# Kernel optimization log

Measured on AMD Instinct MI355X. Metric: run time of the kernel, lower is better.

Reference implementation:

```python
import jax, jax.numpy as jnp
import numpy as np

B, T = 64, 64
HUMAN, IN = 64, 8
HS, ES, K = 1024, 1024, 7
PSI_H, PSI_LR = 1024, 30

_PAR_SHAPES = [(HS, HS), (HS,), (IN, HS), (HS, HUMAN), (IN, HUMAN - IN)]
_PAR_SIZES = [int(np.prod(s)) for s in _PAR_SHAPES]
N_PSI = int(sum(_PAR_SIZES))
_OFFS = np.cumsum([0] + _PAR_SIZES)


def setup_inputs() -> dict:
    key = jax.random.key(0)
    ks = jax.random.split(key, 16)
    def xav(k, shape):
        lim = float(np.sqrt(6.0 / (shape[0] + shape[1])))
        return jax.random.uniform(k, shape, minval=-lim, maxval=lim, dtype=jnp.float32)
    def uni(k, shape, s):
        return jax.random.uniform(k, shape, minval=-s, maxval=s, dtype=jnp.float32)
    se = float(1.0 / np.sqrt(ES))
    return {
        "inputs": jax.random.normal(ks[0], (B, T, IN), jnp.float32),
        "outputs": jax.random.normal(ks[1], (B, T, HUMAN), jnp.float32),
        "eps": jax.random.normal(ks[2], (B, K), jnp.float32),
        "enc_Wih": uni(ks[3], (3 * ES, HUMAN), se),
        "enc_Whh": uni(ks[4], (3 * ES, ES), se),
        "enc_bih": uni(ks[5], (3 * ES,), se),
        "enc_bhh": uni(ks[6], (3 * ES,), se),
        "to_mu": xav(ks[7], (ES, K)),
        "to_lsigma": xav(ks[8], (ES, K)),
        "to_lsigma_bias": -0.5 * jnp.ones((K,), jnp.float32),
        "W1": xav(ks[9], (K, PSI_H)),
        "b1": jnp.zeros((PSI_H,), jnp.float32),
        "W2": xav(ks[10], (PSI_H, PSI_LR)),
        "b2": jnp.zeros((PSI_LR,), jnp.float32),
        "W3": xav(ks[11], (PSI_LR, N_PSI)),
        "b3": jnp.zeros((N_PSI,), jnp.float32),
        "gru_Wih": xav(ks[12], (IN, 2 * HS)),
        "gru_Whh": xav(ks[13], (HS, 2 * HS)),
        "gru_bias": jnp.concatenate([jnp.zeros((HS,)), jnp.ones((HS,))]).astype(jnp.float32),
    }


def _gru_cell(h, x, Wih, Whh, bih, bhh):
    # torch.nn.GRUCell math, gate order (r, z, n)
    gx = x @ Wih.T + bih
    gh = h @ Whh.T + bhh
    xr, xz, xn = jnp.split(gx, 3, axis=-1)
    hr, hz, hn = jnp.split(gh, 3, axis=-1)
    r = jax.nn.sigmoid(xr + hr)
    z = jax.nn.sigmoid(xz + hz)
    n = jnp.tanh(xn + r * hn)
    return (1.0 - z) * n + z * h


def _split_psi(psi):
    # psi: [B, N_PSI] -> per-sample (Whh, bh, Wih, C, D)
    return [psi[:, _OFFS[i]:_OFFS[i + 1]].reshape((-1,) + _PAR_SHAPES[i]) for i in range(5)]


def reference(inputs, outputs, eps, enc_Wih, enc_Whh, enc_bih, enc_bhh,
              to_mu, to_lsigma, to_lsigma_bias, W1, b1, W2, b2, W3, b3,
              gru_Wih, gru_Whh, gru_bias):
    bsz = inputs.shape[0]
    # ---- encoder: GRUCell over time-major outputs ----
    out_tm = jnp.swapaxes(outputs, 0, 1)  # [T, B, HUMAN]
    h0 = jnp.zeros((bsz, ES), inputs.dtype)
    h_enc = _gru_cell(h0, out_tm[0], enc_Wih, enc_Whh, enc_bih, enc_bhh)
    def enc_step(h, x):
        h = _gru_cell(h, x, enc_Wih, enc_Whh, enc_bih, enc_bhh)
        return h, None
    h_enc, _ = jax.lax.scan(enc_step, h_enc, out_tm[1:])
    mu = h_enc @ to_mu                       # [B, K]
    logstd = h_enc @ to_lsigma + to_lsigma_bias
    z = mu + eps * jnp.exp(logstd)
    # ---- hypernetwork psi decoder ----
    psi = (jnp.tanh(z @ W1 + b1) @ W2 + b2) @ W3 + b3   # [B, N_PSI]
    Whh_b, bh_b, Wih_b, C_b, D_b = _split_psi(psi)
    # ---- per-sample GRU decoder, vectorized over batch, scan over time ----
    gx_all = jnp.einsum('bti,ij->tbj', inputs, gru_Wih)  # [T, B, 2*HS]
    xW_all = jnp.einsum('bti,bih->tbh', inputs, Wih_b)   # [T, B, HS]

    def dec_step(h, xs):
        gx_t, xW_t = xs
        pre = gx_t + h @ gru_Whh + gru_bias   # [B, 2*HS]
        z_t = jax.nn.sigmoid(pre[:, :HS])
        r_t = jax.nn.sigmoid(pre[:, HS:])
        hWhh = jnp.einsum('bh,bhk->bk', h, Whh_b) + bh_b
        eta = jnp.tanh(xW_t + r_t * jnp.tanh(hWhh))
        h_new = z_t * h + (1.0 - z_t) * eta
        return h_new, h_new

    state0 = jnp.zeros((bsz, HS), inputs.dtype)
    h_last, dec_seq = jax.lax.scan(dec_step, state0, (gx_all, xW_all))
    dec_seq = jnp.swapaxes(dec_seq, 0, 1)    # [B, T, HS]
    # ---- readout ----
    yhats = jnp.einsum('bth,bhm->btm', dec_seq, C_b)
    xD = jnp.einsum('bti,bim->btm', inputs, D_b)  # [B, T, HUMAN-IN]
    yhats = yhats + jnp.concatenate([jnp.zeros_like(inputs), xD], axis=-1)
    # residual output
    yhats = yhats + jnp.concatenate(
        [inputs, jnp.zeros((bsz, inputs.shape[1], HUMAN - IN), inputs.dtype)], axis=-1)
    states = jax.lax.stop_gradient(h_last)
    return yhats, mu, logstd, states
```

## Files before the change

### kernel.cpp

```cpp
#include <hip/hip_runtime.h>

namespace {
constexpr int nT = 64;
constexpr int nK = 7;
constexpr long N_PSI = 1123776;
constexpr long SZ_WHH = 1048576;
constexpr long REST_SZ = 75200;
constexpr long R_BH = 0;
constexpr long R_WIH = 1024;
constexpr long R_C = 9216;
constexpr long R_D = 74752;
constexpr int NCH = 16;
constexpr int CHR = 64;
constexpr long PHALF = (long)NCH * 64 * 1024;
}

typedef __attribute__((ext_vector_type(4))) unsigned short us4;
typedef __attribute__((ext_vector_type(2))) unsigned short us2;

__device__ __forceinline__ float b2f(unsigned short u) {
  return __uint_as_float(((unsigned int)u) << 16);
}
__device__ __forceinline__ unsigned short f2b(float f) {
  unsigned int u = __float_as_uint(f);
  return (unsigned short)((u + 0x7fffu + ((u >> 16) & 1u)) >> 16);
}
__device__ __forceinline__ float sigm(float x) { return 1.f / (1.f + __expf(-x)); }

__global__ void transpose_bf16_k(const float* __restrict__ in, unsigned short* __restrict__ out,
                                 int rows, int cols) {
  __shared__ float tile[32][33];
  int x = blockIdx.x * 32 + threadIdx.x;
  int y = blockIdx.y * 32 + threadIdx.y;
  #pragma unroll
  for (int i = 0; i < 32; i += 8)
    if ((y + i) < rows && x < cols) tile[threadIdx.y + i][threadIdx.x] = in[(long)(y + i) * cols + x];
  __syncthreads();
  x = blockIdx.y * 32 + threadIdx.x;
  y = blockIdx.x * 32 + threadIdx.y;
  #pragma unroll
  for (int i = 0; i < 32; i += 8)
    if ((y + i) < cols && x < rows) out[(long)(y + i) * rows + x] = f2b(tile[threadIdx.x][threadIdx.y + i]);
}

__global__ void cvt_bf16_k(const float* __restrict__ in, unsigned short* __restrict__ out, long n) {
  long i = (long)blockIdx.x * 256 + threadIdx.x;
  if (i < n) out[i] = f2b(in[i]);
}

__global__ __launch_bounds__(256) void enc_gx_k(const float* __restrict__ outputs,
                                                const unsigned short* __restrict__ WtWihB,
                                                const float* __restrict__ bih,
                                                unsigned short* __restrict__ gxE) {
  int g0 = blockIdx.x * 256;
  int btg = blockIdx.y;
  __shared__ unsigned short ws[64 * 256];
  __shared__ float xs[64][64];
  for (int i = threadIdx.x; i < 64 * 256; i += 256)
    ws[i] = WtWihB[(long)(i >> 8) * 3072 + g0 + (i & 255)];
  for (int i = threadIdx.x; i < 64 * 64; i += 256) {
    int idx = btg * 64 + (i >> 6);
    int t = idx >> 6, b = idx & 63;
    xs[i >> 6][i & 63] = outputs[((long)b * nT + t) * 64 + (i & 63)];
  }
  __syncthreads();
  float bihv = bih[g0 + threadIdx.x];
  for (int j = 0; j < 64; ++j) {
    int idx = btg * 64 + j;
    float acc = bihv;
    #pragma unroll 8
    for (int i = 0; i < 64; ++i) acc += xs[j][i] * b2f(ws[i * 256 + threadIdx.x]);
    gxE[(long)idx * 3072 + g0 + threadIdx.x] = f2b(acc);
  }
}

__global__ __launch_bounds__(256) void dec_gx_k(const float* __restrict__ inputs,
                                                const float* __restrict__ gWih,
                                                const float* __restrict__ gbias,
                                                unsigned short* __restrict__ gxD) {
  int g0 = blockIdx.x * 256;
  int btg = blockIdx.y;
  __shared__ float ws[8][256];
  __shared__ float xs[64][8];
  for (int i = threadIdx.x; i < 8 * 256; i += 256)
    ws[i >> 8][i & 255] = gWih[(long)(i >> 8) * 2048 + g0 + (i & 255)];
  for (int i = threadIdx.x; i < 64 * 8; i += 256) {
    int idx = btg * 64 + (i >> 3);
    int t = idx >> 6, b = idx & 63;
    xs[i >> 3][i & 7] = inputs[((long)b * nT + t) * 8 + (i & 7)];
  }
  __syncthreads();
  float bv = gbias[g0 + threadIdx.x];
  for (int j = 0; j < 64; ++j) {
    int idx = btg * 64 + j;
    float acc = bv;
    #pragma unroll
    for (int i = 0; i < 8; ++i) acc += xs[j][i] * ws[i][threadIdx.x];
    gxD[(long)idx * 2048 + g0 + threadIdx.x] = f2b(acc);
  }
}

__global__ __launch_bounds__(256) void xW_k(const float* __restrict__ inputs,
                                            const float* __restrict__ Rest,
                                            unsigned short* __restrict__ xWb) {
  int k0 = blockIdx.x * 256;
  int b = blockIdx.y;
  __shared__ float ws[8][256];
  __shared__ float xs[64][8];
  const float* RB = Rest + (long)b * REST_SZ + R_WIH;
  for (int i = threadIdx.x; i < 8 * 256; i += 256)
    ws[i >> 8][i & 255] = RB[(long)(i >> 8) * 1024 + k0 + (i & 255)];
  for (int i = threadIdx.x; i < 64 * 8; i += 256)
    xs[i >> 3][i & 7] = inputs[((long)b * nT + (i >> 3)) * 8 + (i & 7)];
  __syncthreads();
  for (int t = 0; t < 64; ++t) {
    float acc = 0.f;
    #pragma unroll
    for (int i = 0; i < 8; ++i) acc += xs[t][i] * ws[i][threadIdx.x];
    xWb[((long)t * 64 + b) * 1024 + k0 + threadIdx.x] = f2b(acc);
  }
}

__global__ __launch_bounds__(256) void enc_step_k(
    const unsigned short* __restrict__ W,
    const unsigned short* __restrict__ gxE,
    const float* __restrict__ bhh,
    float* __restrict__ hEnc,
    const float* __restrict__ pRr, const float* __restrict__ pZr, const float* __restrict__ pNr,
    float* __restrict__ pRw, float* __restrict__ pZw, float* __restrict__ pNw,
    int t) {
  int c = blockIdx.x & (NCH - 1);
  int sp = blockIdx.x >> 4;
  int b0 = sp * 2, b1 = b0 + 1;
  __shared__ float h0s[CHR], h1s[CHR];

  int v = threadIdx.x;
  if (v < 2 * CHR) {
    int hi = v >> 6;
    int bb = hi ? b1 : b0;
    int e = c * CHR + (v & 63);
    float sr = 0.f, sz = 0.f, sn = 0.f;
    if (t > 0) {
      #pragma unroll
      for (int cc = 0; cc < NCH; ++cc) {
        long base = ((long)cc * 64 + bb) * 1024 + e;
        sr += pRr[base]; sz += pZr[base]; sn += pNr[base];
      }
    }
    long gb = ((long)t * 64 + bb) * 3072;
    float xr = b2f(gxE[gb + e]), xz = b2f(gxE[gb + 1024 + e]), xn = b2f(gxE[gb + 2048 + e]);
    float hr = sr + bhh[e], hz = sz + bhh[1024 + e], hn = sn + bhh[2048 + e];
    float r = sigm(xr + hr);
    float z = sigm(xz + hz);
    float n = tanhf(xn + r * hn);
    float hold = (t > 0) ? hEnc[(long)bb * 1024 + e] : 0.f;
    float hnew = (1.f - z) * n + z * hold;
    hEnc[(long)bb * 1024 + e] = hnew;
    if (hi) h1s[v & 63] = hnew; else h0s[v & 63] = hnew;
  }
  __syncthreads();

  if (t < nT - 1) {
    int e0 = threadIdx.x * 4;
    float ar0[4] = {}, az0[4] = {}, an0[4] = {}, ar1[4] = {}, az1[4] = {}, an1[4] = {};
    const unsigned short* Wb = W + (long)(c * CHR) * 3072 + e0;
    #pragma unroll 4
    for (int j = 0; j < CHR; ++j) {
      us4 wr = *(const us4*)(Wb + (long)j * 3072);
      us4 wz = *(const us4*)(Wb + (long)j * 3072 + 1024);
      us4 wn = *(const us4*)(Wb + (long)j * 3072 + 2048);
      float hv0 = h0s[j], hv1 = h1s[j];
      #pragma unroll
      for (int q = 0; q < 4; ++q) {
        float fr = b2f(wr[q]), fz = b2f(wz[q]), fn = b2f(wn[q]);
        ar0[q] += hv0 * fr; az0[q] += hv0 * fz; an0[q] += hv0 * fn;
        ar1[q] += hv1 * fr; az1[q] += hv1 * fz; an1[q] += hv1 * fn;
      }
    }
    long i0 = ((long)c * 64 + b0) * 1024 + e0;
    long i1 = i0 + 1024;
    *(float4*)(pRw + i0) = make_float4(ar0[0], ar0[1], ar0[2], ar0[3]);
    *(float4*)(pZw + i0) = make_float4(az0[0], az0[1], az0[2], az0[3]);
    *(float4*)(pNw + i0) = make_float4(an0[0], an0[1], an0[2], an0[3]);
    *(float4*)(pRw + i1) = make_float4(ar1[0], ar1[1], ar1[2], ar1[3]);
    *(float4*)(pZw + i1) = make_float4(az1[0], az1[1], az1[2], az1[3]);
    *(float4*)(pNw + i1) = make_float4(an1[0], an1[1], an1[2], an1[3]);
  }
}

__global__ __launch_bounds__(256) void latent_hyper_k(
    const float* __restrict__ h_enc,
    const float* __restrict__ to_mu, const float* __restrict__ to_lsig,
    const float* __restrict__ lsig_bias, const float* __restrict__ eps,
    const float* __restrict__ W1, const float* __restrict__ b1,
    const float* __restrict__ W2, const float* __restrict__ b2,
    float* __restrict__ out_mu, float* __restrict__ out_lsig,
    float* __restrict__ a2out) {
  int b = blockIdx.x;
  __shared__ float hs[1024];
  __shared__ float zv[8];
  __shared__ float a1[1024];
  for (int i = threadIdx.x; i < 1024; i += 256) hs[i] = h_enc[b * 1024 + i];
  __syncthreads();
  int g = threadIdx.x >> 5, s = threadIdx.x & 31;
  if (g < nK) {
    float am = 0.f, as_ = 0.f;
    for (int h = s; h < 1024; h += 32) {
      float hv = hs[h];
      am += hv * to_mu[h * nK + g];
      as_ += hv * to_lsig[h * nK + g];
    }
    #pragma unroll
    for (int m = 16; m >= 1; m >>= 1) { am += __shfl_xor(am, m); as_ += __shfl_xor(as_, m); }
    if (s == 0) {
      float ls = as_ + lsig_bias[g];
      out_mu[b * nK + g] = am;
      out_lsig[b * nK + g] = ls;
      zv[g] = am + eps[b * nK + g] * __expf(ls);
    }
  }
  __syncthreads();
  for (int j = threadIdx.x; j < 1024; j += 256) {
    float acc = b1[j];
    #pragma unroll
    for (int i = 0; i < nK; ++i) acc += zv[i] * W1[i * 1024 + j];
    a1[j] = tanhf(acc);
  }
  __syncthreads();
  int l = threadIdx.x >> 3, s8 = threadIdx.x & 7;
  if (l < 30) {
    float acc = 0.f;
    for (int j = s8; j < 1024; j += 8) acc += a1[j] * W2[j * 30 + l];
    acc += __shfl_xor(acc, 4);
    acc += __shfl_xor(acc, 2);
    acc += __shfl_xor(acc, 1);
    if (s8 == 0) a2out[b * 30 + l] = acc + b2[l];
  }
}

__global__ __launch_bounds__(256) void psi_k(const float* __restrict__ a2,
                                             const float* __restrict__ W3, const float* __restrict__ b3,
                                             unsigned short* __restrict__ WhhB, float* __restrict__ Rest) {
  __shared__ float sa[64 * 30];
  for (int i = threadIdx.x; i < 64 * 30; i += 256) sa[i] = a2[i];
  long n0 = ((long)blockIdx.x * 256 + threadIdx.x) * 2;
  __syncthreads();
  if (n0 >= N_PSI) return;
  float2 w[30];
  #pragma unroll
  for (int l = 0; l < 30; ++l) w[l] = *(const float2*)(W3 + (long)l * N_PSI + n0);
  float2 bb = *(const float2*)(b3 + n0);
  bool isWhh = (n0 < SZ_WHH);
  for (int b = 0; b < 64; ++b) {
    float a0 = bb.x, a1v = bb.y;
    const float* ab = &sa[b * 30];
    #pragma unroll
    for (int l = 0; l < 30; ++l) { float av = ab[l]; a0 += av * w[l].x; a1v += av * w[l].y; }
    if (isWhh) {
      us2 o; o[0] = f2b(a0); o[1] = f2b(a1v);
      *(us2*)(WhhB + (long)b * SZ_WHH + n0) = o;
    } else {
      *(float2*)(Rest + (long)b * REST_SZ + (n0 - SZ_WHH)) = make_float2(a0, a1v);
    }
  }
}

__global__ __launch_bounds__(256) void wmax_k(const unsigned short* __restrict__ WhhB,
                                              float* __restrict__ pmax) {
  int b = blockIdx.x >> 2, rq = blockIdx.x & 3;
  int k0 = threadIdx.x * 4;
  float m0 = 0.f, m1 = 0.f, m2 = 0.f, m3 = 0.f;
  const unsigned short* W = WhhB + (long)b * SZ_WHH + (long)rq * 256 * 1024 + k0;
  #pragma unroll 4
  for (int j = 0; j < 256; ++j) {
    us4 w = *(const us4*)(W + (long)j * 1024);
    m0 = fmaxf(m0, fabsf(b2f(w[0])));
    m1 = fmaxf(m1, fabsf(b2f(w[1])));
    m2 = fmaxf(m2, fabsf(b2f(w[2])));
    m3 = fmaxf(m3, fabsf(b2f(w[3])));
  }
  *(float4*)(pmax + ((long)b * 4 + rq) * 1024 + k0) = make_float4(m0, m1, m2, m3);
}

__global__ __launch_bounds__(256) void wscale_k(const float* __restrict__ pmax,
                                                float* __restrict__ wsc) {
  int b = blockIdx.x;
  int k0 = threadIdx.x * 4;
  float4 a = *(const float4*)(pmax + ((long)b * 4 + 0) * 1024 + k0);
  float4 c = *(const float4*)(pmax + ((long)b * 4 + 1) * 1024 + k0);
  float4 d = *(const float4*)(pmax + ((long)b * 4 + 2) * 1024 + k0);
  float4 e = *(const float4*)(pmax + ((long)b * 4 + 3) * 1024 + k0);
  float m0 = fmaxf(fmaxf(a.x, c.x), fmaxf(d.x, e.x));
  float m1 = fmaxf(fmaxf(a.y, c.y), fmaxf(d.y, e.y));
  float m2 = fmaxf(fmaxf(a.z, c.z), fmaxf(d.z, e.z));
  float m3 = fmaxf(fmaxf(a.w, c.w), fmaxf(d.w, e.w));
  float s0 = (m0 > 0.f) ? m0 / 127.f : 1.f;
  float s1 = (m1 > 0.f) ? m1 / 127.f : 1.f;
  float s2 = (m2 > 0.f) ? m2 / 127.f : 1.f;
  float s3 = (m3 > 0.f) ? m3 / 127.f : 1.f;
  *(float4*)(wsc + (long)b * 1024 + k0) = make_float4(s0, s1, s2, s3);
}

__global__ __launch_bounds__(256) void wquant_k(const unsigned short* __restrict__ WhhB,
                                                const float* __restrict__ wsc,
                                                char* __restrict__ Q8) {
  int b = blockIdx.x >> 2, rq = blockIdx.x & 3;
  int k0 = threadIdx.x * 4;
  float4 s = *(const float4*)(wsc + (long)b * 1024 + k0);
  float i0 = 1.f / s.x, i1 = 1.f / s.y, i2 = 1.f / s.z, i3 = 1.f / s.w;
  const unsigned short* W = WhhB + (long)b * SZ_WHH + (long)rq * 256 * 1024 + k0;
  char* Q = Q8 + (long)b * SZ_WHH + (long)rq * 256 * 1024 + k0;
  #pragma unroll 4
  for (int j = 0; j < 256; ++j) {
    us4 w = *(const us4*)(W + (long)j * 1024);
    int q0 = __float2int_rn(b2f(w[0]) * i0);
    int q1 = __float2int_rn(b2f(w[1]) * i1);
    int q2 = __float2int_rn(b2f(w[2]) * i2);
    int q3 = __float2int_rn(b2f(w[3]) * i3);
    q0 = min(127, max(-127, q0)); q1 = min(127, max(-127, q1));
    q2 = min(127, max(-127, q2)); q3 = min(127, max(-127, q3));
    *(char4*)(Q + (long)j * 1024) = make_char4((char)q0, (char)q1, (char)q2, (char)q3);
  }
}

__global__ __launch_bounds__(256) void dec_step_q8_k(
    const char* __restrict__ Q8,
    const float* __restrict__ Wsc,
    const unsigned short* __restrict__ gWhhB,
    const unsigned short* __restrict__ gxD,
    const unsigned short* __restrict__ xWb,
    const float* __restrict__ Rest,
    float* __restrict__ decS,
    const float* __restrict__ pZr, const float* __restrict__ pRr, const float* __restrict__ pWr,
    float* __restrict__ pZw, float* __restrict__ pRw, float* __restrict__ pWw,
    int t) {
  int c = blockIdx.x & (NCH - 1);
  int sp = blockIdx.x >> 4;
  int b0 = sp * 2, b1 = b0 + 1;
  __shared__ float h0s[CHR], h1s[CHR];

  int v = threadIdx.x;
  if (v < 2 * CHR) {
    int hi = v >> 6;
    int bb = hi ? b1 : b0;
    int k = c * CHR + (v & 63);
    float sz = 0.f, sr = 0.f, sw = 0.f;
    float hold = 0.f;
    if (t > 0) {
      #pragma unroll
      for (int cc = 0; cc < NCH; ++cc) {
        long base = ((long)cc * 64 + bb) * 1024 + k;
        sz += pZr[base]; sr += pRr[base]; sw += pWr[base];
      }
      hold = decS[((long)bb * nT + (t - 1)) * 1024 + k];
    }
    long gb = ((long)t * 64 + bb) * 2048;
    float gz = b2f(gxD[gb + k]), gr = b2f(gxD[gb + 1024 + k]);
    float z = sigm(gz + sz);
    float r = sigm(gr + sr);
    float hW = sw + Rest[(long)bb * REST_SZ + R_BH + k];
    float xw = b2f(xWb[((long)t * 64 + bb) * 1024 + k]);
    float eta = tanhf(xw + r * tanhf(hW));
    float hnew = z * hold + (1.f - z) * eta;
    decS[((long)bb * nT + t) * 1024 + k] = hnew;
    if (hi) h1s[v & 63] = hnew; else h0s[v & 63] = hnew;
  }
  __syncthreads();

  if (t < nT - 1) {
    int k0 = threadIdx.x * 4;
    float az0[4] = {}, ar0[4] = {}, aw0[4] = {}, az1[4] = {}, ar1[4] = {}, aw1[4] = {};
    const unsigned short* G = gWhhB + (long)(c * CHR) * 2048 + k0;
    const char* Q0 = Q8 + (long)b0 * SZ_WHH + (long)(c * CHR) * 1024 + k0;
    const char* Q1 = Q8 + (long)b1 * SZ_WHH + (long)(c * CHR) * 1024 + k0;
    #pragma unroll 4
    for (int j = 0; j < CHR; ++j) {
      us4 wz = *(const us4*)(G + (long)j * 2048);
      us4 wr = *(const us4*)(G + (long)j * 2048 + 1024);
      char4 q0 = *(const char4*)(Q0 + (long)j * 1024);
      char4 q1 = *(const char4*)(Q1 + (long)j * 1024);
      float hv0 = h0s[j], hv1 = h1s[j];
      float f00 = (float)q0.x, f01 = (float)q0.y, f02 = (float)q0.z, f03 = (float)q0.w;
      float f10 = (float)q1.x, f11 = (float)q1.y, f12 = (float)q1.z, f13 = (float)q1.w;
      #pragma unroll
      for (int q = 0; q < 4; ++q) {
        float fz = b2f(wz[q]), fr = b2f(wr[q]);
        az0[q] += hv0 * fz; ar0[q] += hv0 * fr;
        az1[q] += hv1 * fz; ar1[q] += hv1 * fr;
      }
      aw0[0] += hv0 * f00; aw0[1] += hv0 * f01; aw0[2] += hv0 * f02; aw0[3] += hv0 * f03;
      aw1[0] += hv1 * f10; aw1[1] += hv1 * f11; aw1[2] += hv1 * f12; aw1[3] += hv1 * f13;
    }
    float4 s0v = *(const float4*)(Wsc + (long)b0 * 1024 + k0);
    float4 s1v = *(const float4*)(Wsc + (long)b1 * 1024 + k0);
    aw0[0] *= s0v.x; aw0[1] *= s0v.y; aw0[2] *= s0v.z; aw0[3] *= s0v.w;
    aw1[0] *= s1v.x; aw1[1] *= s1v.y; aw1[2] *= s1v.z; aw1[3] *= s1v.w;
    long i0 = ((long)c * 64 + b0) * 1024 + k0;
    long i1 = i0 + 1024;
    *(float4*)(pZw + i0) = make_float4(az0[0], az0[1], az0[2], az0[3]);
    *(float4*)(pRw + i0) = make_float4(ar0[0], ar0[1], ar0[2], ar0[3]);
    *(float4*)(pWw + i0) = make_float4(aw0[0], aw0[1], aw0[2], aw0[3]);
    *(float4*)(pZw + i1) = make_float4(az1[0], az1[1], az1[2], az1[3]);
    *(float4*)(pRw + i1) = make_float4(ar1[0], ar1[1], ar1[2], ar1[3]);
    *(float4*)(pWw + i1) = make_float4(aw1[0], aw1[1], aw1[2], aw1[3]);
  }
}

__global__ __launch_bounds__(256) void dec_step_bf_k(
    const unsigned short* __restrict__ WhhB,
    const unsigned short* __restrict__ gWhhB,
    const unsigned short* __restrict__ gxD,
    const unsigned short* __restrict__ xWb,
    const float* __restrict__ Rest,
    float* __restrict__ decS,
    const float* __restrict__ pZr, const float* __restrict__ pRr, const float* __restrict__ pWr,
    float* __restrict__ pZw, float* __restrict__ pRw, float* __restrict__ pWw,
    int t) {
  int c = blockIdx.x & (NCH - 1);
  int sp = blockIdx.x >> 4;
  int b0 = sp * 2, b1 = b0 + 1;
  __shared__ float h0s[CHR], h1s[CHR];

  int v = threadIdx.x;
  if (v < 2 * CHR) {
    int hi = v >> 6;
    int bb = hi ? b1 : b0;
    int k = c * CHR + (v & 63);
    float sz = 0.f, sr = 0.f, sw = 0.f;
    float hold = 0.f;
    if (t > 0) {
      #pragma unroll
      for (int cc = 0; cc < NCH; ++cc) {
        long base = ((long)cc * 64 + bb) * 1024 + k;
        sz += pZr[base]; sr += pRr[base]; sw += pWr[base];
      }
      hold = decS[((long)bb * nT + (t - 1)) * 1024 + k];
    }
    long gb = ((long)t * 64 + bb) * 2048;
    float gz = b2f(gxD[gb + k]), gr = b2f(gxD[gb + 1024 + k]);
    float z = sigm(gz + sz);
    float r = sigm(gr + sr);
    float hW = sw + Rest[(long)bb * REST_SZ + R_BH + k];
    float xw = b2f(xWb[((long)t * 64 + bb) * 1024 + k]);
    float eta = tanhf(xw + r * tanhf(hW));
    float hnew = z * hold + (1.f - z) * eta;
    decS[((long)bb * nT + t) * 1024 + k] = hnew;
    if (hi) h1s[v & 63] = hnew; else h0s[v & 63] = hnew;
  }
  __syncthreads();

  if (t < nT - 1) {
    int k0 = threadIdx.x * 4;
    float az0[4] = {}, ar0[4] = {}, aw0[4] = {}, az1[4] = {}, ar1[4] = {}, aw1[4] = {};
    const unsigned short* G = gWhhB + (long)(c * CHR) * 2048 + k0;
    const unsigned short* W0 = WhhB + (long)b0 * SZ_WHH + (long)(c * CHR) * 1024 + k0;
    const unsigned short* W1p = WhhB + (long)b1 * SZ_WHH + (long)(c * CHR) * 1024 + k0;
    #pragma unroll 4
    for (int j = 0; j < CHR; ++j) {
      us4 wz = *(const us4*)(G + (long)j * 2048);
      us4 wr = *(const us4*)(G + (long)j * 2048 + 1024);
      us4 w0 = *(const us4*)(W0 + (long)j * 1024);
      us4 w1 = *(const us4*)(W1p + (long)j * 1024);
      float hv0 = h0s[j], hv1 = h1s[j];
      #pragma unroll
      for (int q = 0; q < 4; ++q) {
        float fz = b2f(wz[q]), fr = b2f(wr[q]), f0 = b2f(w0[q]), f1 = b2f(w1[q]);
        az0[q] += hv0 * fz; ar0[q] += hv0 * fr; aw0[q] += hv0 * f0;
        az1[q] += hv1 * fz; ar1[q] += hv1 * fr; aw1[q] += hv1 * f1;
      }
    }
    long i0 = ((long)c * 64 + b0) * 1024 + k0;
    long i1 = i0 + 1024;
    *(float4*)(pZw + i0) = make_float4(az0[0], az0[1], az0[2], az0[3]);
    *(float4*)(pRw + i0) = make_float4(ar0[0], ar0[1], ar0[2], ar0[3]);
    *(float4*)(pWw + i0) = make_float4(aw0[0], aw0[1], aw0[2], aw0[3]);
    *(float4*)(pZw + i1) = make_float4(az1[0], az1[1], az1[2], az1[3]);
    *(float4*)(pRw + i1) = make_float4(ar1[0], ar1[1], ar1[2], ar1[3]);
    *(float4*)(pWw + i1) = make_float4(aw1[0], aw1[1], aw1[2], aw1[3]);
  }
}

__global__ __launch_bounds__(256) void readout_k(
    const float* __restrict__ dec_seq, const float* __restrict__ inputs,
    const float* __restrict__ Rest, float* __restrict__ yhats) {
  int b = blockIdx.x >> 3;
  int tg = blockIdx.x & 7;
  __shared__ float ss[8][1024];
  __shared__ float part[4][8][64];
  for (int i = threadIdx.x; i < 8 * 1024; i += 256)
    ss[i >> 10][i & 1023] = dec_seq[((long)b * nT + tg * 8 + (i >> 10)) * 1024 + (i & 1023)];
  __syncthreads();
  int m = threadIdx.x & 63, hq = threadIdx.x >> 6;
  const float* C = Rest + (long)b * REST_SZ + R_C;
  float acc[8] = {};
  for (int h = hq * 256; h < hq * 256 + 256; ++h) {
    float cv = C[(long)h * 64 + m];
    #pragma unroll
    for (int tt = 0; tt < 8; ++tt) acc[tt] += ss[tt][h] * cv;
  }
  #pragma unroll
  for (int tt = 0; tt < 8; ++tt) part[hq][tt][m] = acc[tt];
  __syncthreads();
  const float* D = Rest + (long)b * REST_SZ + R_D;
  for (int o = threadIdx.x; o < 512; o += 256) {
    int tt = o >> 6, mm = o & 63;
    float a = part[0][tt][mm] + part[1][tt][mm] + part[2][tt][mm] + part[3][tt][mm];
    long bt = (long)b * nT + tg * 8 + tt;
    if (mm < 8) {
      a += inputs[bt * 8 + mm];
    } else {
      #pragma unroll
      for (int i = 0; i < 8; ++i) a += inputs[bt * 8 + i] * D[i * 56 + (mm - 8)];
    }
    yhats[bt * 64 + mm] = a;
  }
}

__global__ void copy_states_k(const float* __restrict__ dec_seq, float* __restrict__ states) {
  int i = blockIdx.x * 256 + threadIdx.x;
  int b = i >> 10, h = i & 1023;
  states[i] = dec_seq[((long)b * nT + (nT - 1)) * 1024 + h];
}

extern "C" void kernel_launch(void* const* d_in, const int* in_sizes, int n_in,
                              void* d_out, int out_size, void* d_ws, size_t ws_size,
                              hipStream_t stream) {
  const float* inputs  = (const float*)d_in[0];
  const float* outputs = (const float*)d_in[1];
  const float* eps     = (const float*)d_in[2];
  const float* enc_Wih = (const float*)d_in[3];
  const float* enc_Whh = (const float*)d_in[4];
  const float* enc_bih = (const float*)d_in[5];
  const float* enc_bhh = (const float*)d_in[6];
  const float* to_mu   = (const float*)d_in[7];
  const float* to_lsig = (const float*)d_in[8];
  const float* lsig_b  = (const float*)d_in[9];
  const float* W1 = (const float*)d_in[10];
  const float* b1 = (const float*)d_in[11];
  const float* W2 = (const float*)d_in[12];
  const float* b2 = (const float*)d_in[13];
  const float* W3 = (const float*)d_in[14];
  const float* b3 = (const float*)d_in[15];
  const float* gWih  = (const float*)d_in[16];
  const float* gWhh  = (const float*)d_in[17];
  const float* gbias = (const float*)d_in[18];

  char* ws = (char*)d_ws;
  size_t off = 0;
  auto alloc = [&](size_t bytes) { size_t o = off; off = (off + bytes + 255) & ~(size_t)255; return o; };
  size_t oWhhB   = alloc(64ull * SZ_WHH * 2);
  size_t oRest   = alloc(64ull * REST_SZ * 4);
  size_t ogWhhB  = alloc(1024ull * 2048 * 2);
  size_t oWtWhhB = alloc(1024ull * 3072 * 2);
  size_t oWtWihB = alloc(64ull * 3072 * 2);
  size_t ogxE    = alloc(64ull * 64 * 3072 * 2);
  size_t ogxD    = alloc(64ull * 64 * 2048 * 2);
  size_t oxWb    = alloc(64ull * 64 * 1024 * 2);
  size_t opA     = alloc((size_t)2 * PHALF * 4);
  size_t opB     = alloc((size_t)2 * PHALF * 4);
  size_t opC     = alloc((size_t)2 * PHALF * 4);
  size_t ohA     = alloc(64ull * 1024 * 4);
  size_t oDec    = alloc(64ull * 64 * 1024 * 4);
  size_t oA2     = alloc(64 * 30 * 4);
  size_t oQ8     = alloc(64ull * SZ_WHH);
  size_t oPmax   = alloc(64ull * 4 * 1024 * 4);
  size_t oWsc    = alloc(64ull * 1024 * 4);
  bool useQ8 = (off <= ws_size);
  (void)in_sizes; (void)n_in; (void)out_size;

  unsigned short* WhhB   = (unsigned short*)(ws + oWhhB);
  float*          Rest   = (float*)(ws + oRest);
  unsigned short* gWhhB  = (unsigned short*)(ws + ogWhhB);
  unsigned short* WtWhhB = (unsigned short*)(ws + oWtWhhB);
  unsigned short* WtWihB = (unsigned short*)(ws + oWtWihB);
  unsigned short* gxE    = (unsigned short*)(ws + ogxE);
  unsigned short* gxD    = (unsigned short*)(ws + ogxD);
  unsigned short* xWb    = (unsigned short*)(ws + oxWb);
  float* pA   = (float*)(ws + opA);
  float* pB   = (float*)(ws + opB);
  float* pC   = (float*)(ws + opC);
  float* hA   = (float*)(ws + ohA);
  float* decS = (float*)(ws + oDec);
  float* a2   = (float*)(ws + oA2);
  char*  Q8   = (char*)(ws + oQ8);
  float* pmax = (float*)(ws + oPmax);
  float* wsc  = (float*)(ws + oWsc);

  float* out    = (float*)d_out;
  float* out_yh = out;
  float* out_mu = out + 262144;
  float* out_ls = out + 262144 + 448;
  float* out_st = out + 262144 + 896;

  transpose_bf16_k<<<dim3(32, 96), dim3(32, 8), 0, stream>>>(enc_Whh, WtWhhB, 3072, 1024);
  transpose_bf16_k<<<dim3(2, 96),  dim3(32, 8), 0, stream>>>(enc_Wih, WtWihB, 3072, 64);
  cvt_bf16_k<<<(int)((1024ull * 2048 + 255) / 256), 256, 0, stream>>>(gWhh, gWhhB, 1024 * 2048);

  enc_gx_k<<<dim3(12, 64), 256, 0, stream>>>(outputs, WtWihB, enc_bih, gxE);

  for (int t = 0; t < nT; ++t) {
    int rp = t & 1, wp = (t + 1) & 1;
    enc_step_k<<<512, 256, 0, stream>>>(WtWhhB, gxE, enc_bhh, hA,
        pA + (size_t)rp * PHALF, pB + (size_t)rp * PHALF, pC + (size_t)rp * PHALF,
        pA + (size_t)wp * PHALF, pB + (size_t)wp * PHALF, pC + (size_t)wp * PHALF, t);
  }

  latent_hyper_k<<<64, 256, 0, stream>>>(hA, to_mu, to_lsig, lsig_b, eps,
                                         W1, b1, W2, b2, out_mu, out_ls, a2);
  psi_k<<<(int)((N_PSI / 2 + 255) / 256), 256, 0, stream>>>(a2, W3, b3, WhhB, Rest);

  if (useQ8) {
    wmax_k<<<256, 256, 0, stream>>>(WhhB, pmax);
    wscale_k<<<64, 256, 0, stream>>>(pmax, wsc);
    wquant_k<<<256, 256, 0, stream>>>(WhhB, wsc, Q8);
  }

  dec_gx_k<<<dim3(8, 64), 256, 0, stream>>>(inputs, gWih, gbias, gxD);
  xW_k<<<dim3(4, 64), 256, 0, stream>>>(inputs, Rest, xWb);

  for (int t = 0; t < nT; ++t) {
    int rp = t & 1, wp = (t + 1) & 1;
    if (useQ8) {
      dec_step_q8_k<<<512, 256, 0, stream>>>(Q8, wsc, gWhhB, gxD, xWb, Rest, decS,
          pA + (size_t)rp * PHALF, pB + (size_t)rp * PHALF, pC + (size_t)rp * PHALF,
          pA + (size_t)wp * PHALF, pB + (size_t)wp * PHALF, pC + (size_t)wp * PHALF, t);
    } else {
      dec_step_bf_k<<<512, 256, 0, stream>>>(WhhB, gWhhB, gxD, xWb, Rest, decS,
          pA + (size_t)rp * PHALF, pB + (size_t)rp * PHALF, pC + (size_t)rp * PHALF,
          pA + (size_t)wp * PHALF, pB + (size_t)wp * PHALF, pC + (size_t)wp * PHALF, t);
    }
  }

  readout_k<<<512, 256, 0, stream>>>(decS, inputs, Rest, out_yh);
  copy_states_k<<<256, 256, 0, stream>>>(decS, out_st);
}
```

Measured before the change: 2.989 ms.

## Double per-step block size, splitting gate matvecs and partial-sum reduction across threads

The encoder and decoder recurrent step kernels go from 256 to 512 threads per block. The cross-chunk partial-sum reduction is now spread over four thread groups and combined through shared memory. The matvec work is split so one half of the threads computes the r/z gates and the other half computes the n/W gate. This gives more parallelism and memory-level concurrency in these latency-bound per-timestep launches, at the cost of an extra barrier. The workspace is also reordered so the Q8 buffer is allocated last, which can let the int8 path be taken when the workspace is only just large enough.

```diff
diff --git a/kernel.cpp b/kernel.cpp
--- a/kernel.cpp
+++ b/kernel.cpp
@@ -11,7 +11,6 @@
 constexpr long R_C = 9216;
 constexpr long R_D = 74752;
 constexpr int NCH = 16;
-constexpr int CHR = 64;
 constexpr long PHALF = (long)NCH * 64 * 1024;
 }
 
@@ -121,7 +120,7 @@
   }
 }
 
-__global__ __launch_bounds__(256) void enc_step_k(
+__global__ __launch_bounds__(512, 2) void enc_step3_k(
     const unsigned short* __restrict__ W,
     const unsigned short* __restrict__ gxE,
     const float* __restrict__ bhh,
@@ -132,21 +131,31 @@
   int c = blockIdx.x & (NCH - 1);
   int sp = blockIdx.x >> 4;
   int b0 = sp * 2, b1 = b0 + 1;
-  __shared__ float h0s[CHR], h1s[CHR];
-
+  __shared__ float h0s[64], h1s[64];
+  __shared__ float red[3][4][128];
   int v = threadIdx.x;
-  if (v < 2 * CHR) {
-    int hi = v >> 6;
-    int bb = hi ? b1 : b0;
-    int e = c * CHR + (v & 63);
+  {
+    int q = v >> 7, idx = v & 127;
+    int bb = (idx >> 6) ? b1 : b0;
+    int e = c * 64 + (idx & 63);
     float sr = 0.f, sz = 0.f, sn = 0.f;
     if (t > 0) {
       #pragma unroll
-      for (int cc = 0; cc < NCH; ++cc) {
+      for (int cc = q * 4; cc < q * 4 + 4; ++cc) {
         long base = ((long)cc * 64 + bb) * 1024 + e;
         sr += pRr[base]; sz += pZr[base]; sn += pNr[base];
       }
     }
+    red[0][q][idx] = sr; red[1][q][idx] = sz; red[2][q][idx] = sn;
+  }
+  __syncthreads();
+  if (v < 128) {
+    int hi = v >> 6;
+    int bb = hi ? b1 : b0;
+    int e = c * 64 + (v & 63);
+    float sr = red[0][0][v] + red[0][1][v] + red[0][2][v] + red[0][3][v];
+    float sz = red[1][0][v] + red[1][1][v] + red[1][2][v] + red[1][3][v];
+    float sn = red[2][0][v] + red[2][1][v] + red[2][2][v] + red[2][3][v];
     long gb = ((long)t * 64 + bb) * 3072;
     float xr = b2f(gxE[gb + e]), xz = b2f(gxE[gb + 1024 + e]), xn = b2f(gxE[gb + 2048 + e]);
     float hr = sr + bhh[e], hz = sz + bhh[1024 + e], hn = sn + bhh[2048 + e];
@@ -159,32 +168,48 @@
     if (hi) h1s[v & 63] = hnew; else h0s[v & 63] = hnew;
   }
   __syncthreads();
-
   if (t < nT - 1) {
-    int e0 = threadIdx.x * 4;
-    float ar0[4] = {}, az0[4] = {}, an0[4] = {}, ar1[4] = {}, az1[4] = {}, an1[4] = {};
-    const unsigned short* Wb = W + (long)(c * CHR) * 3072 + e0;
-    #pragma unroll 4
-    for (int j = 0; j < CHR; ++j) {
-      us4 wr = *(const us4*)(Wb + (long)j * 3072);
-      us4 wz = *(const us4*)(Wb + (long)j * 3072 + 1024);
-      us4 wn = *(const us4*)(Wb + (long)j * 3072 + 2048);
-      float hv0 = h0s[j], hv1 = h1s[j];
-      #pragma unroll
-      for (int q = 0; q < 4; ++q) {
-        float fr = b2f(wr[q]), fz = b2f(wz[q]), fn = b2f(wn[q]);
-        ar0[q] += hv0 * fr; az0[q] += hv0 * fz; an0[q] += hv0 * fn;
-        ar1[q] += hv1 * fr; az1[q] += hv1 * fz; an1[q] += hv1 * fn;
-      }
-    }
-    long i0 = ((long)c * 64 + b0) * 1024 + e0;
-    long i1 = i0 + 1024;
-    *(float4*)(pRw + i0) = make_float4(ar0[0], ar0[1], ar0[2], ar0[3]);
-    *(float4*)(pZw + i0) = make_float4(az0[0], az0[1], az0[2], az0[3]);
-    *(float4*)(pNw + i0) = make_float4(an0[0], an0[1], an0[2], an0[3]);
-    *(float4*)(pRw + i1) = make_float4(ar1[0], ar1[1], ar1[2], ar1[3]);
-    *(float4*)(pZw + i1) = make_float4(az1[0], az1[1], az1[2], az1[3]);
-    *(float4*)(pNw + i1) = make_float4(an1[0], an1[1], an1[2], an1[3]);
+    if (v < 256) {
+      int e0 = v * 4;
+      float ar0[4] = {}, az0[4] = {}, ar1[4] = {}, az1[4] = {};
+      const unsigned short* Wb = W + (long)(c * 64) * 3072 + e0;
+      #pragma unroll 4
+      for (int j = 0; j < 64; ++j) {
+        us4 wr = *(const us4*)(Wb + (long)j * 3072);
+        us4 wz = *(const us4*)(Wb + (long)j * 3072 + 1024);
+        float hv0 = h0s[j], hv1 = h1s[j];
+        #pragma unroll
+        for (int q = 0; q < 4; ++q) {
+          float fr = b2f(wr[q]), fz = b2f(wz[q]);
+          ar0[q] += hv0 * fr; az0[q] += hv0 * fz;
+          ar1[q] += hv1 * fr; az1[q] += hv1 * fz;
+        }
+      }
+      long i0 = ((long)c * 64 + b0) * 1024 + e0;
+      long i1 = i0 + 1024;
+      *(float4*)(pRw + i0) = make_float4(ar0[0], ar0[1], ar0[2], ar0[3]);
+      *(float4*)(pZw + i0) = make_float4(az0[0], az0[1], az0[2], az0[3]);
+      *(float4*)(pRw + i1) = make_float4(ar1[0], ar1[1], ar1[2], ar1[3]);
+      *(float4*)(pZw + i1) = make_float4(az1[0], az1[1], az1[2], az1[3]);
+    } else {
+      int e0 = (v - 256) * 4;
+      float an0[4] = {}, an1[4] = {};
+      const unsigned short* Wb = W + (long)(c * 64) * 3072 + 2048 + e0;
+      #pragma unroll 8
+      for (int j = 0; j < 64; ++j) {
+        us4 wn = *(const us4*)(Wb + (long)j * 3072);
+        float hv0 = h0s[j], hv1 = h1s[j];
+        #pragma unroll
+        for (int q = 0; q < 4; ++q) {
+          float fn = b2f(wn[q]);
+          an0[q] += hv0 * fn; an1[q] += hv1 * fn;
+        }
+      }
+      long i0 = ((long)c * 64 + b0) * 1024 + e0;
+      long i1 = i0 + 1024;
+      *(float4*)(pNw + i0) = make_float4(an0[0], an0[1], an0[2], an0[3]);
+      *(float4*)(pNw + i1) = make_float4(an1[0], an1[1], an1[2], an1[3]);
+    }
   }
 }
 
@@ -323,7 +348,7 @@
   }
 }
 
-__global__ __launch_bounds__(256) void dec_step_q8_k(
+__global__ __launch_bounds__(512, 2) void dec_step_q8e_k(
     const char* __restrict__ Q8,
     const float* __restrict__ Wsc,
     const unsigned short* __restrict__ gWhhB,
@@ -337,23 +362,31 @@
   int c = blockIdx.x & (NCH - 1);
   int sp = blockIdx.x >> 4;
   int b0 = sp * 2, b1 = b0 + 1;
-  __shared__ float h0s[CHR], h1s[CHR];
-
+  __shared__ float h0s[64], h1s[64];
+  __shared__ float red[3][4][128];
   int v = threadIdx.x;
-  if (v < 2 * CHR) {
+  {
+    int q = v >> 7, idx = v & 127;
+    int bb = (idx >> 6) ? b1 : b0;
+    int k = c * 64 + (idx & 63);
+    float sz = 0.f, sr = 0.f, sw = 0.f;
+    if (t > 0) {
+      #pragma unroll
+      for (int cc = q * 4; cc < q * 4 + 4; ++cc) {
+        long base = ((long)cc * 64 + bb) * 1024 + k;
+        sz += pZr[base]; sr += pRr[base]; sw += pWr[base];
+      }
+    }
+    red[0][q][idx] = sz; red[1][q][idx] = sr; red[2][q][idx] = sw;
+  }
+  __syncthreads();
+  if (v < 128) {
     int hi = v >> 6;
     int bb = hi ? b1 : b0;
-    int k = c * CHR + (v & 63);
-    float sz = 0.f, sr = 0.f, sw = 0.f;
-    float hold = 0.f;
-    if (t > 0) {
-      #pragma unroll
-      for (int cc = 0; cc < NCH; ++cc) {
-        long base = ((long)cc * 64 + bb) * 1024 + k;
-        sz += pZr[base]; sr += pRr[base]; sw += pWr[base];
-      }
-      hold = decS[((long)bb * nT + (t - 1)) * 1024 + k];
-    }
+    int k = c * 64 + (v & 63);
+    float sz = red[0][0][v] + red[0][1][v] + red[0][2][v] + red[0][3][v];
+    float sr = red[1][0][v] + red[1][1][v] + red[1][2][v] + red[1][3][v];
+    float sw = red[2][0][v] + red[2][1][v] + red[2][2][v] + red[2][3][v];
     long gb = ((long)t * 64 + bb) * 2048;
     float gz = b2f(gxD[gb + k]), gr = b2f(gxD[gb + 1024 + k]);
     float z = sigm(gz + sz);
@@ -361,52 +394,63 @@
     float hW = sw + Rest[(long)bb * REST_SZ + R_BH + k];
     float xw = b2f(xWb[((long)t * 64 + bb) * 1024 + k]);
     float eta = tanhf(xw + r * tanhf(hW));
+    float hold = (t > 0) ? decS[((long)bb * nT + (t - 1)) * 1024 + k] : 0.f;
     float hnew = z * hold + (1.f - z) * eta;
     decS[((long)bb * nT + t) * 1024 + k] = hnew;
     if (hi) h1s[v & 63] = hnew; else h0s[v & 63] = hnew;
   }
   __syncthreads();
-
   if (t < nT - 1) {
-    int k0 = threadIdx.x * 4;
-    float az0[4] = {}, ar0[4] = {}, aw0[4] = {}, az1[4] = {}, ar1[4] = {}, aw1[4] = {};
-    const unsigned short* G = gWhhB + (long)(c * CHR) * 2048 + k0;
-    const char* Q0 = Q8 + (long)b0 * SZ_WHH + (long)(c * CHR) * 1024 + k0;
-    const char* Q1 = Q8 + (long)b1 * SZ_WHH + (long)(c * CHR) * 1024 + k0;
-    #pragma unroll 4
-    for (int j = 0; j < CHR; ++j) {
-      us4 wz = *(const us4*)(G + (long)j * 2048);
-      us4 wr = *(const us4*)(G + (long)j * 2048 + 1024);
-      char4 q0 = *(const char4*)(Q0 + (long)j * 1024);
-      char4 q1 = *(const char4*)(Q1 + (long)j * 1024);
-      float hv0 = h0s[j], hv1 = h1s[j];
-      float f00 = (float)q0.x, f01 = (float)q0.y, f02 = (float)q0.z, f03 = (float)q0.w;
-      float f10 = (float)q1.x, f11 = (float)q1.y, f12 = (float)q1.z, f13 = (float)q1.w;
-      #pragma unroll
-      for (int q = 0; q < 4; ++q) {
-        float fz = b2f(wz[q]), fr = b2f(wr[q]);
-        az0[q] += hv0 * fz; ar0[q] += hv0 * fr;
-        az1[q] += hv1 * fz; ar1[q] += hv1 * fr;
-      }
-      aw0[0] += hv0 * f00; aw0[1] += hv0 * f01; aw0[2] += hv0 * f02; aw0[3] += hv0 * f03;
-      aw1[0] += hv1 * f10; aw1[1] += hv1 * f11; aw1[2] += hv1 * f12; aw1[3] += hv1 * f13;
-    }
-    float4 s0v = *(const float4*)(Wsc + (long)b0 * 1024 + k0);
-    float4 s1v = *(const float4*)(Wsc + (long)b1 * 1024 + k0);
-    aw0[0] *= s0v.x; aw0[1] *= s0v.y; aw0[2] *= s0v.z; aw0[3] *= s0v.w;
-    aw1[0] *= s1v.x; aw1[1] *= s1v.y; aw1[2] *= s1v.z; aw1[3] *= s1v.w;
-    long i0 = ((long)c * 64 + b0) * 1024 + k0;
-    long i1 = i0 + 1024;
-    *(float4*)(pZw + i0) = make_float4(az0[0], az0[1], az0[2], az0[3]);
-    *(float4*)(pRw + i0) = make_float4(ar0[0], ar0[1], ar0[2], ar0[3]);
-    *(float4*)(pWw + i0) = make_float4(aw0[0], aw0[1], aw0[2], aw0[3]);
-    *(float4*)(pZw + i1) = make_float4(az1[0], az1[1], az1[2], az1[3]);
-    *(float4*)(pRw + i1) = make_float4(ar1[0], ar1[1], ar1[2], ar1[3]);
-    *(float4*)(pWw + i1) = make_float4(aw1[0], aw1[1], aw1[2], aw1[3]);
-  }
-}
-
-__global__ __launch_bounds__(256) void dec_step_bf_k(
+    if (v < 256) {
+      int k0 = v * 4;
+      float az0[4] = {}, ar0[4] = {}, az1[4] = {}, ar1[4] = {};
+      const unsigned short* G = gWhhB + (long)(c * 64) * 2048 + k0;
+      #pragma unroll 4
+      for (int j = 0; j < 64; ++j) {
+        us4 wz = *(const us4*)(G + (long)j * 2048);
+        us4 wr = *(const us4*)(G + (long)j * 2048 + 1024);
+        float hv0 = h0s[j], hv1 = h1s[j];
+        #pragma unroll
+        for (int q = 0; q < 4; ++q) {
+          float fz = b2f(wz[q]), fr = b2f(wr[q]);
+          az0[q] += hv0 * fz; ar0[q] += hv0 * fr;
+          az1[q] += hv1 * fz; ar1[q] += hv1 * fr;
+        }
+      }
+      long i0 = ((long)c * 64 + b0) * 1024 + k0;
+      long i1 = i0 + 1024;
+      *(float4*)(pZw + i0) = make_float4(az0[0], az0[1], az0[2], az0[3]);
+      *(float4*)(pRw + i0) = make_float4(ar0[0], ar0[1], ar0[2], ar0[3]);
+      *(float4*)(pZw + i1) = make_float4(az1[0], az1[1], az1[2], az1[3]);
+      *(float4*)(pRw + i1) = make_float4(ar1[0], ar1[1], ar1[2], ar1[3]);
+    } else {
+      int k0 = (v - 256) * 4;
+      float aw0[4] = {}, aw1[4] = {};
+      const char* Q0 = Q8 + (long)b0 * SZ_WHH + (long)(c * 64) * 1024 + k0;
+      const char* Q1 = Q8 + (long)b1 * SZ_WHH + (long)(c * 64) * 1024 + k0;
+      #pragma unroll 8
+      for (int j = 0; j < 64; ++j) {
+        char4 q0 = *(const char4*)(Q0 + (long)j * 1024);
+        char4 q1 = *(const char4*)(Q1 + (long)j * 1024);
+        float hv0 = h0s[j], hv1 = h1s[j];
+        aw0[0] += hv0 * (float)q0.x; aw0[1] += hv0 * (float)q0.y;
+        aw0[2] += hv0 * (float)q0.z; aw0[3] += hv0 * (float)q0.w;
+        aw1[0] += hv1 * (float)q1.x; aw1[1] += hv1 * (float)q1.y;
+        aw1[2] += hv1 * (float)q1.z; aw1[3] += hv1 * (float)q1.w;
+      }
+      float4 s0v = *(const float4*)(Wsc + (long)b0 * 1024 + k0);
+      float4 s1v = *(const float4*)(Wsc + (long)b1 * 1024 + k0);
+      aw0[0] *= s0v.x; aw0[1] *= s0v.y; aw0[2] *= s0v.z; aw0[3] *= s0v.w;
+      aw1[0] *= s1v.x; aw1[1] *= s1v.y; aw1[2] *= s1v.z; aw1[3] *= s1v.w;
+      long i0 = ((long)c * 64 + b0) * 1024 + k0;
+      long i1 = i0 + 1024;
+      *(float4*)(pWw + i0) = make_float4(aw0[0], aw0[1], aw0[2], aw0[3]);
+      *(float4*)(pWw + i1) = make_float4(aw1[0], aw1[1], aw1[2], aw1[3]);
+    }
+  }
+}
+
+__global__ __launch_bounds__(512, 2) void dec_step_bf3_k(
     const unsigned short* __restrict__ WhhB,
     const unsigned short* __restrict__ gWhhB,
     const unsigned short* __restrict__ gxD,
@@ -419,23 +463,31 @@
   int c = blockIdx.x & (NCH - 1);
   int sp = blockIdx.x >> 4;
   int b0 = sp * 2, b1 = b0 + 1;
-  __shared__ float h0s[CHR], h1s[CHR];
-
+  __shared__ float h0s[64], h1s[64];
+  __shared__ float red[3][4][128];
   int v = threadIdx.x;
-  if (v < 2 * CHR) {
+  {
+    int q = v >> 7, idx = v & 127;
+    int bb = (idx >> 6) ? b1 : b0;
+    int k = c * 64 + (idx & 63);
+    float sz = 0.f, sr = 0.f, sw = 0.f;
+    if (t > 0) {
+      #pragma unroll
+      for (int cc = q * 4; cc < q * 4 + 4; ++cc) {
+        long base = ((long)cc * 64 + bb) * 1024 + k;
+        sz += pZr[base]; sr += pRr[base]; sw += pWr[base];
+      }
+    }
+    red[0][q][idx] = sz; red[1][q][idx] = sr; red[2][q][idx] = sw;
+  }
+  __syncthreads();
+  if (v < 128) {
     int hi = v >> 6;
     int bb = hi ? b1 : b0;
-    int k = c * CHR + (v & 63);
-    float sz = 0.f, sr = 0.f, sw = 0.f;
-    float hold = 0.f;
-    if (t > 0) {
-      #pragma unroll
-      for (int cc = 0; cc < NCH; ++cc) {
-        long base = ((long)cc * 64 + bb) * 1024 + k;
-        sz += pZr[base]; sr += pRr[base]; sw += pWr[base];
-      }
-      hold = decS[((long)bb * nT + (t - 1)) * 1024 + k];
-    }
+    int k = c * 64 + (v & 63);
+    float sz = red[0][0][v] + red[0][1][v] + red[0][2][v] + red[0][3][v];
+    float sr = red[1][0][v] + red[1][1][v] + red[1][2][v] + red[1][3][v];
+    float sw = red[2][0][v] + red[2][1][v] + red[2][2][v] + red[2][3][v];
     long gb = ((long)t * 64 + bb) * 2048;
     float gz = b2f(gxD[gb + k]), gr = b2f(gxD[gb + 1024 + k]);
     float z = sigm(gz + sz);
@@ -443,40 +495,56 @@
     float hW = sw + Rest[(long)bb * REST_SZ + R_BH + k];
     float xw = b2f(xWb[((long)t * 64 + bb) * 1024 + k]);
     float eta = tanhf(xw + r * tanhf(hW));
+    float hold = (t > 0) ? decS[((long)bb * nT + (t - 1)) * 1024 + k] : 0.f;
     float hnew = z * hold + (1.f - z) * eta;
     decS[((long)bb * nT + t) * 1024 + k] = hnew;
     if (hi) h1s[v & 63] = hnew; else h0s[v & 63] = hnew;
   }
   __syncthreads();
-
   if (t < nT - 1) {
-    int k0 = threadIdx.x * 4;
-    float az0[4] = {}, ar0[4] = {}, aw0[4] = {}, az1[4] = {}, ar1[4] = {}, aw1[4] = {};
-    const unsigned short* G = gWhhB + (long)(c * CHR) * 2048 + k0;
-    const unsigned short* W0 = WhhB + (long)b0 * SZ_WHH + (long)(c * CHR) * 1024 + k0;
-    const unsigned short* W1p = WhhB + (long)b1 * SZ_WHH + (long)(c * CHR) * 1024 + k0;
-    #pragma unroll 4
-    for (int j = 0; j < CHR; ++j) {
-      us4 wz = *(const us4*)(G + (long)j * 2048);
-      us4 wr = *(const us4*)(G + (long)j * 2048 + 1024);
-      us4 w0 = *(const us4*)(W0 + (long)j * 1024);
-      us4 w1 = *(const us4*)(W1p + (long)j * 1024);
-      float hv0 = h0s[j], hv1 = h1s[j];
-      #pragma unroll
-      for (int q = 0; q < 4; ++q) {
-        float fz = b2f(wz[q]), fr = b2f(wr[q]), f0 = b2f(w0[q]), f1 = b2f(w1[q]);
-        az0[q] += hv0 * fz; ar0[q] += hv0 * fr; aw0[q] += hv0 * f0;
-        az1[q] += hv1 * fz; ar1[q] += hv1 * fr; aw1[q] += hv1 * f1;
-      }
-    }
-    long i0 = ((long)c * 64 + b0) * 1024 + k0;
-    long i1 = i0 + 1024;
-    *(float4*)(pZw + i0) = make_float4(az0[0], az0[1], az0[2], az0[3]);
-    *(float4*)(pRw + i0) = make_float4(ar0[0], ar0[1], ar0[2], ar0[3]);
-    *(float4*)(pWw + i0) = make_float4(aw0[0], aw0[1], aw0[2], aw0[3]);
-    *(float4*)(pZw + i1) = make_float4(az1[0], az1[1], az1[2], az1[3]);
-    *(float4*)(pRw + i1) = make_float4(ar1[0], ar1[1], ar1[2], ar1[3]);
-    *(float4*)(pWw + i1) = make_float4(aw1[0], aw1[1], aw1[2], aw1[3]);
+    if (v < 256) {
+      int k0 = v * 4;
+      float az0[4] = {}, ar0[4] = {}, az1[4] = {}, ar1[4] = {};
+      const unsigned short* G = gWhhB + (long)(c * 64) * 2048 + k0;
+      #pragma unroll 4
+      for (int j = 0; j < 64; ++j) {
+        us4 wz = *(const us4*)(G + (long)j * 2048);
+        us4 wr = *(const us4*)(G + (long)j * 2048 + 1024);
+        float hv0 = h0s[j], hv1 = h1s[j];
+        #pragma unroll
+        for (int q = 0; q < 4; ++q) {
+          float fz = b2f(wz[q]), fr = b2f(wr[q]);
+          az0[q] += hv0 * fz; ar0[q] += hv0 * fr;
+          az1[q] += hv1 * fz; ar1[q] += hv1 * fr;
+        }
+      }
+      long i0 = ((long)c * 64 + b0) * 1024 + k0;
+      long i1 = i0 + 1024;
+      *(float4*)(pZw + i0) = make_float4(az0[0], az0[1], az0[2], az0[3]);
+      *(float4*)(pRw + i0) = make_float4(ar0[0], ar0[1], ar0[2], ar0[3]);
+      *(float4*)(pZw + i1) = make_float4(az1[0], az1[1], az1[2], az1[3]);
+      *(float4*)(pRw + i1) = make_float4(ar1[0], ar1[1], ar1[2], ar1[3]);
+    } else {
+      int k0 = (v - 256) * 4;
+      float aw0[4] = {}, aw1[4] = {};
+      const unsigned short* W0 = WhhB + (long)b0 * SZ_WHH + (long)(c * 64) * 1024 + k0;
+      const unsigned short* W1p = WhhB + (long)b1 * SZ_WHH + (long)(c * 64) * 1024 + k0;
+      #pragma unroll 8
+      for (int j = 0; j < 64; ++j) {
+        us4 w0 = *(const us4*)(W0 + (long)j * 1024);
+        us4 w1 = *(const us4*)(W1p + (long)j * 1024);
+        float hv0 = h0s[j], hv1 = h1s[j];
+        #pragma unroll
+        for (int q = 0; q < 4; ++q) {
+          aw0[q] += hv0 * b2f(w0[q]);
+          aw1[q] += hv1 * b2f(w1[q]);
+        }
+      }
+      long i0 = ((long)c * 64 + b0) * 1024 + k0;
+      long i1 = i0 + 1024;
+      *(float4*)(pWw + i0) = make_float4(aw0[0], aw0[1], aw0[2], aw0[3]);
+      *(float4*)(pWw + i1) = make_float4(aw1[0], aw1[1], aw1[2], aw1[3]);
+    }
   }
 }
 
@@ -548,8 +616,8 @@
   char* ws = (char*)d_ws;
   size_t off = 0;
   auto alloc = [&](size_t bytes) { size_t o = off; off = (off + bytes + 255) & ~(size_t)255; return o; };
+  size_t oRest   = alloc(64ull * REST_SZ * 4);
   size_t oWhhB   = alloc(64ull * SZ_WHH * 2);
-  size_t oRest   = alloc(64ull * REST_SZ * 4);
   size_t ogWhhB  = alloc(1024ull * 2048 * 2);
   size_t oWtWhhB = alloc(1024ull * 3072 * 2);
   size_t oWtWihB = alloc(64ull * 3072 * 2);
@@ -562,14 +630,14 @@
   size_t ohA     = alloc(64ull * 1024 * 4);
   size_t oDec    = alloc(64ull * 64 * 1024 * 4);
   size_t oA2     = alloc(64 * 30 * 4);
-  size_t oQ8     = alloc(64ull * SZ_WHH);
   size_t oPmax   = alloc(64ull * 4 * 1024 * 4);
   size_t oWsc    = alloc(64ull * 1024 * 4);
+  size_t oQ8     = alloc(64ull * SZ_WHH);
   bool useQ8 = (off <= ws_size);
   (void)in_sizes; (void)n_in; (void)out_size;
 
+  float*          Rest   = (float*)(ws + oRest);
   unsigned short* WhhB   = (unsigned short*)(ws + oWhhB);
-  float*          Rest   = (float*)(ws + oRest);
   unsigned short* gWhhB  = (unsigned short*)(ws + ogWhhB);
   unsigned short* WtWhhB = (unsigned short*)(ws + oWtWhhB);
   unsigned short* WtWihB = (unsigned short*)(ws + oWtWihB);
@@ -582,9 +650,9 @@
   float* hA   = (float*)(ws + ohA);
   float* decS = (float*)(ws + oDec);
   float* a2   = (float*)(ws + oA2);
-  char*  Q8   = (char*)(ws + oQ8);
   float* pmax = (float*)(ws + oPmax);
   float* wsc  = (float*)(ws + oWsc);
+  char*  Q8   = (char*)(ws + oQ8);
 
   float* out    = (float*)d_out;
   float* out_yh = out;
@@ -600,7 +668,7 @@
 
   for (int t = 0; t < nT; ++t) {
     int rp = t & 1, wp = (t + 1) & 1;
-    enc_step_k<<<512, 256, 0, stream>>>(WtWhhB, gxE, enc_bhh, hA,
+    enc_step3_k<<<512, 512, 0, stream>>>(WtWhhB, gxE, enc_bhh, hA,
         pA + (size_t)rp * PHALF, pB + (size_t)rp * PHALF, pC + (size_t)rp * PHALF,
         pA + (size_t)wp * PHALF, pB + (size_t)wp * PHALF, pC + (size_t)wp * PHALF, t);
   }
@@ -608,7 +676,6 @@
   latent_hyper_k<<<64, 256, 0, stream>>>(hA, to_mu, to_lsig, lsig_b, eps,
                                          W1, b1, W2, b2, out_mu, out_ls, a2);
   psi_k<<<(int)((N_PSI / 2 + 255) / 256), 256, 0, stream>>>(a2, W3, b3, WhhB, Rest);
-
   if (useQ8) {
     wmax_k<<<256, 256, 0, stream>>>(WhhB, pmax);
     wscale_k<<<64, 256, 0, stream>>>(pmax, wsc);
@@ -621,11 +688,11 @@
   for (int t = 0; t < nT; ++t) {
     int rp = t & 1, wp = (t + 1) & 1;
     if (useQ8) {
-      dec_step_q8_k<<<512, 256, 0, stream>>>(Q8, wsc, gWhhB, gxD, xWb, Rest, decS,
+      dec_step_q8e_k<<<512, 512, 0, stream>>>(Q8, wsc, gWhhB, gxD, xWb, Rest, decS,
           pA + (size_t)rp * PHALF, pB + (size_t)rp * PHALF, pC + (size_t)rp * PHALF,
           pA + (size_t)wp * PHALF, pB + (size_t)wp * PHALF, pC + (size_t)wp * PHALF, t);
     } else {
-      dec_step_bf_k<<<512, 256, 0, stream>>>(WhhB, gWhhB, gxD, xWb, Rest, decS,
+      dec_step_bf3_k<<<512, 512, 0, stream>>>(WhhB, gWhhB, gxD, xWb, Rest, decS,
           pA + (size_t)rp * PHALF, pB + (size_t)rp * PHALF, pC + (size_t)rp * PHALF,
           pA + (size_t)wp * PHALF, pB + (size_t)wp * PHALF, pC + (size_t)wp * PHALF, t);
     }
```

Result: faster. 2.814 ms (-5.8%).
